# Kernel tuning notes

Hardware: AMD Instinct MI355X
Metric: run time of the kernel (lower is better)

## Reference

```python
import jax, jax.numpy as jnp
import numpy as np

INPUT_DIM = 512
OUTPUT_DIM = 512
NUM_BASIS = 16
GRID_MIN, GRID_MAX = -2.0, 2.0
LN_EPS = 1e-5


def rbf_basis(x):
    # x: [batch, input_dim] -> [batch, input_dim, num_basis]
    centers = jnp.linspace(GRID_MIN, GRID_MAX, NUM_BASIS, dtype=x.dtype)  # [K]
    h = (GRID_MAX - GRID_MIN) / (NUM_BASIS - 1)
    z = (x[..., None] - centers) / h
    return jnp.exp(-(z * z))


def setup_inputs() -> dict:
    key = jax.random.key(0)
    k1, k2, k3 = jax.random.split(key, 3)
    x = jax.random.normal(k1, (4096, INPUT_DIM), dtype=jnp.float32)
    weights = jax.random.normal(k2, (OUTPUT_DIM, INPUT_DIM, NUM_BASIS), dtype=jnp.float32) * 0.1
    base_weights = jax.random.normal(k3, (OUTPUT_DIM, INPUT_DIM), dtype=jnp.float32) * 0.1
    ln_gamma = jnp.ones((OUTPUT_DIM,), dtype=jnp.float32)
    ln_beta = jnp.zeros((OUTPUT_DIM,), dtype=jnp.float32)
    return {"x": x, "weights": weights, "base_weights": base_weights,
            "ln_gamma": ln_gamma, "ln_beta": ln_beta}


def reference(x, weights, base_weights, ln_gamma, ln_beta):
    # per-edge basis expansion: [B, I, K]
    basis = rbf_basis(x)
    # fused contraction replacing the nested python loops:
    # out[b, j] = sum_{i,k} basis[b, i, k] * weights[j, i, k]
    out = jnp.einsum('bik,jik->bj', basis, weights)
    # residual base activation path
    out = out + jax.nn.silu(x) @ base_weights.T
    # layer norm over output_dim
    mean = jnp.mean(out, axis=-1, keepdims=True)
    var = jnp.var(out, axis=-1, keepdims=True)
    out = (out - mean) * jax.lax.rsqrt(var + LN_EPS) * ln_gamma + ln_beta
    return out
```

## Files before the change

kernel.cpp:

```cpp
#include <hip/hip_runtime.h>
#include <hip/hip_bf16.h>


typedef __bf16 bf16x8 __attribute__((ext_vector_type(8)));
typedef __bf16 bf16x4 __attribute__((ext_vector_type(4)));
typedef float  f32x4  __attribute__((ext_vector_type(4)));

#define KT 8704
#define SPLITS 8
#define KS (KT / SPLITS)
#define NT2 (KS / 64)
#define CPE (4096 * 512)
#define ATILE (256 * 64)

__device__ __forceinline__ void gll16(const __bf16* g, __bf16* l) {
    __builtin_amdgcn_global_load_lds(
        (const __attribute__((address_space(1))) void*)g,
        (__attribute__((address_space(3))) void*)l, 16, 0, 0);
}

__global__ void prep_AB(const float* __restrict__ x, const float* __restrict__ W,
                        const float* __restrict__ Wb, __bf16* __restrict__ Asilu,
                        __bf16* __restrict__ B) {
    if (blockIdx.x < 1024) {
        int t = blockIdx.x * 256 + threadIdx.x;
        int e = t * 8;
        float4 v0 = *(const float4*)&x[e];
        float4 v1 = *(const float4*)&x[e + 4];
        float vs[8] = {v0.x, v0.y, v0.z, v0.w, v1.x, v1.y, v1.z, v1.w};
        bf16x8 o;
#pragma unroll
        for (int j = 0; j < 8; ++j) o[j] = (__bf16)(vs[j] / (1.0f + __expf(-vs[j])));
        *(bf16x8*)&Asilu[e] = o;
    } else {
        int t = (blockIdx.x - 1024) * 256 + threadIdx.x;
        int j = t / 2176;
        int c = (t - j * 2176) * 4;
        float4 v;
        if (c < 8192) v = *(const float4*)&W[(size_t)j * 8192 + c];
        else          v = *(const float4*)&Wb[(size_t)j * 512 + (c - 8192)];
        bf16x4 o;
        o[0] = (__bf16)v.x; o[1] = (__bf16)v.y; o[2] = (__bf16)v.z; o[3] = (__bf16)v.w;
        *(bf16x4*)&B[(size_t)j * KT + c] = o;
    }
}

__global__ __launch_bounds__(512, 2) void gemm_bt(const float* __restrict__ xg,
                                                  const __bf16* __restrict__ Sg,
                                                  const __bf16* __restrict__ B,
                                                  __bf16* __restrict__ Cp) {
    __shared__ __attribute__((aligned(16))) __bf16 As[2 * ATILE];
    __shared__ __attribute__((aligned(16))) __bf16 Bs[2 * ATILE];

    const int tid  = threadIdx.x;
    const int wave = tid >> 6, lane = tid & 63;
    const int q    = lane >> 4, r16 = lane & 15;
    const int m0 = blockIdx.x * 256, n0 = blockIdx.y * 256, k0 = blockIdx.z * KS;
    const int wm = wave >> 2, wn = wave & 3;

    const int sr = tid >> 3;
    const int sc = (tid & 7) ^ ((tid >> 4) & 7);
    const __bf16* gB0 = B + (size_t)(n0 + sr) * KT       + k0 + sc * 8;
    const __bf16* gB1 = B + (size_t)(n0 + 64  + sr) * KT + k0 + sc * 8;
    const __bf16* gB2 = B + (size_t)(n0 + 128 + sr) * KT + k0 + sc * 8;
    const __bf16* gB3 = B + (size_t)(n0 + 192 + sr) * KT + k0 + sc * 8;
    const __bf16* gS0 = Sg + (size_t)(m0 + sr) * 512       + sc * 8;
    const __bf16* gS1 = Sg + (size_t)(m0 + 64  + sr) * 512 + sc * 8;
    const __bf16* gS2 = Sg + (size_t)(m0 + 128 + sr) * 512 + sc * 8;
    const __bf16* gS3 = Sg + (size_t)(m0 + 192 + sr) * 512 + sc * 8;
    const float* xp0 = xg + (size_t)(m0 + sr) * 512       + (sc >> 1);
    const float* xp1 = xg + (size_t)(m0 + 64  + sr) * 512 + (sc >> 1);
    const float* xp2 = xg + (size_t)(m0 + 128 + sr) * 512 + (sc >> 1);
    const float* xp3 = xg + (size_t)(m0 + 192 + sr) * 512 + (sc >> 1);
    const float j0f  = (float)(8 * (sc & 1));

    f32x4 acc[8][4] = {};

    const int swl = (r16 >> 1) & 7;
    const int qx0 = ((q)     ^ swl) * 8;
    const int qx1 = ((4 + q) ^ swl) * 8;
    const int aro = (wm * 128 + r16) * 64;
    const int bro = (wn * 64  + r16) * 64;

    auto basis8 = [&](float xv) -> bf16x8 {
        const float zc = 3.75f * xv + 7.5f - j0f;
        bf16x8 o;
#pragma unroll
        for (int d = 0; d < 8; ++d) { float z = zc - (float)d; o[d] = (__bf16)__expf(-z * z); }
        return o;
    };

    float xA, xB, xC, xD;
    {
        const int xo = k0 >> 4;
        float x0 = xp0[xo], x1 = xp1[xo], x2 = xp2[xo], x3 = xp3[xo];
        gll16(gB0, &Bs[(size_t)tid * 8]);
        gll16(gB1, &Bs[(size_t)(512 + tid) * 8]);
        gll16(gB2, &Bs[(size_t)(1024 + tid) * 8]);
        gll16(gB3, &Bs[(size_t)(1536 + tid) * 8]);
        *(bf16x8*)(As + (size_t)tid * 8)          = basis8(x0);
        *(bf16x8*)(As + (size_t)(512 + tid) * 8)  = basis8(x1);
        *(bf16x8*)(As + (size_t)(1024 + tid) * 8) = basis8(x2);
        *(bf16x8*)(As + (size_t)(1536 + tid) * 8) = basis8(x3);
        const int xo1 = (k0 + 64) >> 4;
        xA = xp0[xo1]; xB = xp1[xo1]; xC = xp2[xo1]; xD = xp3[xo1];
    }
    __syncthreads();

    bf16x8 a[8], b[4];
    for (int u = 0; u < NT2; ++u) {
        const int s   = u & 1;
        const int cbo = s * ATILE;
        const int so1 = (s ^ 1) * ATILE;
        const int k1  = (u + 1) * 64;
        const int kn  = k0 + k1;
        const bool nb = kn < 8192;
        const int kk  = kn - 8192;
        const int k2g = kn + 64;
        const bool nb2 = k2g < 8192;
        float t0, t1, t2, t3;

#pragma unroll
        for (int mi = 0; mi < 8; ++mi) a[mi] = *(const bf16x8*)(As + cbo + aro + mi * 1024 + qx0);
#pragma unroll
        for (int ni = 0; ni < 4; ++ni) b[ni] = *(const bf16x8*)(Bs + cbo + bro + ni * 1024 + qx0);
        gll16(gB0 + k1, &Bs[(size_t)(so1 + tid * 8)]);
        gll16(gB1 + k1, &Bs[(size_t)(so1 + (512 + tid) * 8)]);
        gll16(gB2 + k1, &Bs[(size_t)(so1 + (1024 + tid) * 8)]);
        gll16(gB3 + k1, &Bs[(size_t)(so1 + (1536 + tid) * 8)]);
        if (nb) {
            *(bf16x8*)(As + so1 + (size_t)tid * 8)          = basis8(xA);
            *(bf16x8*)(As + so1 + (size_t)(1024 + tid) * 8) = basis8(xC);
        } else {
            gll16(gS0 + kk, &As[(size_t)(so1 + tid * 8)]);
            gll16(gS1 + kk, &As[(size_t)(so1 + (512 + tid) * 8)]);
            gll16(gS2 + kk, &As[(size_t)(so1 + (1024 + tid) * 8)]);
            gll16(gS3 + kk, &As[(size_t)(so1 + (1536 + tid) * 8)]);
        }
        if (nb2) {
            const int xo = k2g >> 4;
            t0 = xp0[xo]; t1 = xp1[xo]; t2 = xp2[xo]; t3 = xp3[xo];
        }
        __builtin_amdgcn_s_setprio(1);
#pragma unroll
        for (int mi = 0; mi < 8; ++mi)
#pragma unroll
            for (int ni = 0; ni < 4; ++ni)
                acc[mi][ni] = __builtin_amdgcn_mfma_f32_16x16x32_bf16(a[mi], b[ni], acc[mi][ni], 0, 0, 0);
        __builtin_amdgcn_s_setprio(0);
        __builtin_amdgcn_s_barrier();

#pragma unroll
        for (int mi = 0; mi < 8; ++mi) a[mi] = *(const bf16x8*)(As + cbo + aro + mi * 1024 + qx1);
#pragma unroll
        for (int ni = 0; ni < 4; ++ni) b[ni] = *(const bf16x8*)(Bs + cbo + bro + ni * 1024 + qx1);
        if (nb) {
            *(bf16x8*)(As + so1 + (size_t)(512 + tid) * 8)  = basis8(xB);
            *(bf16x8*)(As + so1 + (size_t)(1536 + tid) * 8) = basis8(xD);
        }
        __builtin_amdgcn_s_setprio(1);
#pragma unroll
        for (int mi = 0; mi < 8; ++mi)
#pragma unroll
            for (int ni = 0; ni < 4; ++ni)
                acc[mi][ni] = __builtin_amdgcn_mfma_f32_16x16x32_bf16(a[mi], b[ni], acc[mi][ni], 0, 0, 0);
        __builtin_amdgcn_s_setprio(0);
        if (nb2) { xA = t0; xB = t1; xC = t2; xD = t3; }
        __syncthreads();
    }

    __bf16* Cb = Cp + (size_t)blockIdx.z * CPE;
#pragma unroll
    for (int mi = 0; mi < 8; ++mi) {
        const int row = m0 + wm * 128 + mi * 16 + q * 4;
#pragma unroll
        for (int ni = 0; ni < 4; ++ni) {
            const int col = n0 + wn * 64 + ni * 16 + r16;
#pragma unroll
            for (int r = 0; r < 4; ++r)
                Cb[(size_t)(row + r) * 512 + col] = (__bf16)acc[mi][ni][r];
        }
    }
}

__global__ void ln_kernel(const __bf16* __restrict__ Cp, const float* __restrict__ gamma,
                          const float* __restrict__ beta, float* __restrict__ out) {
    const int tid  = threadIdx.x;
    const int wave = tid >> 6, lane = tid & 63;
    const int row  = blockIdx.x * 4 + wave;
    const size_t base = (size_t)row * 512 + lane * 8;

    float v[8] = {};
    float s = 0.f, s2 = 0.f;
#pragma unroll
    for (int z = 0; z < SPLITS; ++z) {
        bf16x8 p = *(const bf16x8*)(Cp + (size_t)z * CPE + base);
#pragma unroll
        for (int j = 0; j < 8; ++j) v[j] += (float)p[j];
    }
#pragma unroll
    for (int j = 0; j < 8; ++j) { s += v[j]; s2 += v[j] * v[j]; }
#pragma unroll
    for (int m = 32; m >= 1; m >>= 1) {
        s  += __shfl_xor(s, m);
        s2 += __shfl_xor(s2, m);
    }
    const float mean = s * (1.0f / 512.0f);
    const float var  = s2 * (1.0f / 512.0f) - mean * mean;
    const float rs   = rsqrtf(var + 1e-5f);
    float4 o0, o1;
    const float4 g0 = *(const float4*)&gamma[lane * 8];
    const float4 g1 = *(const float4*)&gamma[lane * 8 + 4];
    const float4 b0 = *(const float4*)&beta[lane * 8];
    const float4 b1 = *(const float4*)&beta[lane * 8 + 4];
    o0.x = (v[0] - mean) * rs * g0.x + b0.x;
    o0.y = (v[1] - mean) * rs * g0.y + b0.y;
    o0.z = (v[2] - mean) * rs * g0.z + b0.z;
    o0.w = (v[3] - mean) * rs * g0.w + b0.w;
    o1.x = (v[4] - mean) * rs * g1.x + b1.x;
    o1.y = (v[5] - mean) * rs * g1.y + b1.y;
    o1.z = (v[6] - mean) * rs * g1.z + b1.z;
    o1.w = (v[7] - mean) * rs * g1.w + b1.w;
    *(float4*)&out[base]     = o0;
    *(float4*)&out[base + 4] = o1;
}

extern "C" void kernel_launch(void* const* d_in, const int* in_sizes, int n_in,
                              void* d_out, int out_size, void* d_ws, size_t ws_size,
                              hipStream_t stream) {
    const float* x     = (const float*)d_in[0];
    const float* W     = (const float*)d_in[1];
    const float* Wb    = (const float*)d_in[2];
    const float* gamma = (const float*)d_in[3];
    const float* beta  = (const float*)d_in[4];
    float* out = (float*)d_out;

    char* ws = (char*)d_ws;
    __bf16* Asilu = (__bf16*)ws;
    __bf16* Bm    = (__bf16*)(ws + 4194304);
    __bf16* Cp    = (__bf16*)(ws + 13107200);

    prep_AB<<<1024 + 4352, 256, 0, stream>>>(x, W, Wb, Asilu, Bm);
    dim3 g(16, 2, SPLITS);
    gemm_bt<<<g, 512, 0, stream>>>(x, Asilu, Bm, Cp);
    ln_kernel<<<1024, 256, 0, stream>>>(Cp, gamma, beta, out);
}
```

Baseline: 129.6 us.

## Fuse SiLU computation into GEMM A-tile loading and drop precomputed SiLU buffer

The prep kernel no longer writes a bf16 SiLU copy of x. The GEMM instead loads fp32 x directly for the last 512 K columns and computes SiLU while staging the A tile into shared memory. The intra-iteration schedule also changes: the mid-iteration barrier is removed, and all A-tile writes move after the second-half fragment loads. This saves a kernel pass and a workspace round trip, at the cost of extra register pressure and exp work inside the GEMM. Dropping the barrier may be unsafe if other waves still read the buffer being overwritten.

```diff
diff --git a/kernel.cpp b/kernel.cpp
--- a/kernel.cpp
+++ b/kernel.cpp
@@ -19,34 +19,20 @@
         (__attribute__((address_space(3))) void*)l, 16, 0, 0);
 }
 
-__global__ void prep_AB(const float* __restrict__ x, const float* __restrict__ W,
-                        const float* __restrict__ Wb, __bf16* __restrict__ Asilu,
-                        __bf16* __restrict__ B) {
-    if (blockIdx.x < 1024) {
-        int t = blockIdx.x * 256 + threadIdx.x;
-        int e = t * 8;
-        float4 v0 = *(const float4*)&x[e];
-        float4 v1 = *(const float4*)&x[e + 4];
-        float vs[8] = {v0.x, v0.y, v0.z, v0.w, v1.x, v1.y, v1.z, v1.w};
-        bf16x8 o;
-#pragma unroll
-        for (int j = 0; j < 8; ++j) o[j] = (__bf16)(vs[j] / (1.0f + __expf(-vs[j])));
-        *(bf16x8*)&Asilu[e] = o;
-    } else {
-        int t = (blockIdx.x - 1024) * 256 + threadIdx.x;
-        int j = t / 2176;
-        int c = (t - j * 2176) * 4;
-        float4 v;
-        if (c < 8192) v = *(const float4*)&W[(size_t)j * 8192 + c];
-        else          v = *(const float4*)&Wb[(size_t)j * 512 + (c - 8192)];
-        bf16x4 o;
-        o[0] = (__bf16)v.x; o[1] = (__bf16)v.y; o[2] = (__bf16)v.z; o[3] = (__bf16)v.w;
-        *(bf16x4*)&B[(size_t)j * KT + c] = o;
-    }
+__global__ void prep_B(const float* __restrict__ W, const float* __restrict__ Wb,
+                       __bf16* __restrict__ B) {
+    int t = blockIdx.x * 256 + threadIdx.x;
+    int j = t / 2176;
+    int c = (t - j * 2176) * 4;
+    float4 v;
+    if (c < 8192) v = *(const float4*)&W[(size_t)j * 8192 + c];
+    else          v = *(const float4*)&Wb[(size_t)j * 512 + (c - 8192)];
+    bf16x4 o;
+    o[0] = (__bf16)v.x; o[1] = (__bf16)v.y; o[2] = (__bf16)v.z; o[3] = (__bf16)v.w;
+    *(bf16x4*)&B[(size_t)j * KT + c] = o;
 }
 
 __global__ __launch_bounds__(512, 2) void gemm_bt(const float* __restrict__ xg,
-                                                  const __bf16* __restrict__ Sg,
                                                   const __bf16* __restrict__ B,
                                                   __bf16* __restrict__ Cp) {
     __shared__ __attribute__((aligned(16))) __bf16 As[2 * ATILE];
@@ -64,15 +50,12 @@
     const __bf16* gB1 = B + (size_t)(n0 + 64  + sr) * KT + k0 + sc * 8;
     const __bf16* gB2 = B + (size_t)(n0 + 128 + sr) * KT + k0 + sc * 8;
     const __bf16* gB3 = B + (size_t)(n0 + 192 + sr) * KT + k0 + sc * 8;
-    const __bf16* gS0 = Sg + (size_t)(m0 + sr) * 512       + sc * 8;
-    const __bf16* gS1 = Sg + (size_t)(m0 + 64  + sr) * 512 + sc * 8;
-    const __bf16* gS2 = Sg + (size_t)(m0 + 128 + sr) * 512 + sc * 8;
-    const __bf16* gS3 = Sg + (size_t)(m0 + 192 + sr) * 512 + sc * 8;
-    const float* xp0 = xg + (size_t)(m0 + sr) * 512       + (sc >> 1);
-    const float* xp1 = xg + (size_t)(m0 + 64  + sr) * 512 + (sc >> 1);
-    const float* xp2 = xg + (size_t)(m0 + 128 + sr) * 512 + (sc >> 1);
-    const float* xp3 = xg + (size_t)(m0 + 192 + sr) * 512 + (sc >> 1);
-    const float j0f  = (float)(8 * (sc & 1));
+    const float* xs0 = xg + (size_t)(m0 + sr) * 512;
+    const float* xs1 = xg + (size_t)(m0 + 64  + sr) * 512;
+    const float* xs2 = xg + (size_t)(m0 + 128 + sr) * 512;
+    const float* xs3 = xg + (size_t)(m0 + 192 + sr) * 512;
+    const int   xco = sc >> 1;
+    const float j0f = (float)(8 * (sc & 1));
 
     f32x4 acc[8][4] = {};
 
@@ -89,11 +72,18 @@
         for (int d = 0; d < 8; ++d) { float z = zc - (float)d; o[d] = (__bf16)__expf(-z * z); }
         return o;
     };
+    auto silu8 = [&](float4 va, float4 vb) -> bf16x8 {
+        float v[8] = {va.x, va.y, va.z, va.w, vb.x, vb.y, vb.z, vb.w};
+        bf16x8 o;
+#pragma unroll
+        for (int d = 0; d < 8; ++d) o[d] = (__bf16)(v[d] / (1.0f + __expf(-v[d])));
+        return o;
+    };
 
     float xA, xB, xC, xD;
     {
-        const int xo = k0 >> 4;
-        float x0 = xp0[xo], x1 = xp1[xo], x2 = xp2[xo], x3 = xp3[xo];
+        const int xo = (k0 >> 4) + xco;
+        float x0 = xs0[xo], x1 = xs1[xo], x2 = xs2[xo], x3 = xs3[xo];
         gll16(gB0, &Bs[(size_t)tid * 8]);
         gll16(gB1, &Bs[(size_t)(512 + tid) * 8]);
         gll16(gB2, &Bs[(size_t)(1024 + tid) * 8]);
@@ -102,8 +92,8 @@
         *(bf16x8*)(As + (size_t)(512 + tid) * 8)  = basis8(x1);
         *(bf16x8*)(As + (size_t)(1024 + tid) * 8) = basis8(x2);
         *(bf16x8*)(As + (size_t)(1536 + tid) * 8) = basis8(x3);
-        const int xo1 = (k0 + 64) >> 4;
-        xA = xp0[xo1]; xB = xp1[xo1]; xC = xp2[xo1]; xD = xp3[xo1];
+        const int xo1 = ((k0 + 64) >> 4) + xco;
+        xA = xs0[xo1]; xB = xs1[xo1]; xC = xs2[xo1]; xD = xs3[xo1];
     }
     __syncthreads();
 
@@ -115,10 +105,11 @@
         const int k1  = (u + 1) * 64;
         const int kn  = k0 + k1;
         const bool nb = kn < 8192;
-        const int kk  = kn - 8192;
+        const int kk  = (kn - 8192 > 448) ? 448 : (kn - 8192);
         const int k2g = kn + 64;
         const bool nb2 = k2g < 8192;
         float t0, t1, t2, t3;
+        float4 sa0, sa1, sb0, sb1, sc0, sc1, sd0, sd1;
 
 #pragma unroll
         for (int mi = 0; mi < 8; ++mi) a[mi] = *(const bf16x8*)(As + cbo + aro + mi * 1024 + qx0);
@@ -128,35 +119,39 @@
         gll16(gB1 + k1, &Bs[(size_t)(so1 + (512 + tid) * 8)]);
         gll16(gB2 + k1, &Bs[(size_t)(so1 + (1024 + tid) * 8)]);
         gll16(gB3 + k1, &Bs[(size_t)(so1 + (1536 + tid) * 8)]);
+        if (!nb) {
+            const int col = kk + sc * 8;
+            sa0 = *(const float4*)(xs0 + col); sa1 = *(const float4*)(xs0 + col + 4);
+            sb0 = *(const float4*)(xs1 + col); sb1 = *(const float4*)(xs1 + col + 4);
+            sc0 = *(const float4*)(xs2 + col); sc1 = *(const float4*)(xs2 + col + 4);
+            sd0 = *(const float4*)(xs3 + col); sd1 = *(const float4*)(xs3 + col + 4);
+        }
+        if (nb2) {
+            const int xo = (k2g >> 4) + xco;
+            t0 = xs0[xo]; t1 = xs1[xo]; t2 = xs2[xo]; t3 = xs3[xo];
+        }
+        __builtin_amdgcn_s_setprio(1);
+#pragma unroll
+        for (int mi = 0; mi < 8; ++mi)
+#pragma unroll
+            for (int ni = 0; ni < 4; ++ni)
+                acc[mi][ni] = __builtin_amdgcn_mfma_f32_16x16x32_bf16(a[mi], b[ni], acc[mi][ni], 0, 0, 0);
+        __builtin_amdgcn_s_setprio(0);
+
+#pragma unroll
+        for (int mi = 0; mi < 8; ++mi) a[mi] = *(const bf16x8*)(As + cbo + aro + mi * 1024 + qx1);
+#pragma unroll
+        for (int ni = 0; ni < 4; ++ni) b[ni] = *(const bf16x8*)(Bs + cbo + bro + ni * 1024 + qx1);
         if (nb) {
             *(bf16x8*)(As + so1 + (size_t)tid * 8)          = basis8(xA);
             *(bf16x8*)(As + so1 + (size_t)(1024 + tid) * 8) = basis8(xC);
-        } else {
-            gll16(gS0 + kk, &As[(size_t)(so1 + tid * 8)]);
-            gll16(gS1 + kk, &As[(size_t)(so1 + (512 + tid) * 8)]);
-            gll16(gS2 + kk, &As[(size_t)(so1 + (1024 + tid) * 8)]);
-            gll16(gS3 + kk, &As[(size_t)(so1 + (1536 + tid) * 8)]);
-        }
-        if (nb2) {
-            const int xo = k2g >> 4;
-            t0 = xp0[xo]; t1 = xp1[xo]; t2 = xp2[xo]; t3 = xp3[xo];
-        }
-        __builtin_amdgcn_s_setprio(1);
-#pragma unroll
-        for (int mi = 0; mi < 8; ++mi)
-#pragma unroll
-            for (int ni = 0; ni < 4; ++ni)
-                acc[mi][ni] = __builtin_amdgcn_mfma_f32_16x16x32_bf16(a[mi], b[ni], acc[mi][ni], 0, 0, 0);
-        __builtin_amdgcn_s_setprio(0);
-        __builtin_amdgcn_s_barrier();
-
-#pragma unroll
-        for (int mi = 0; mi < 8; ++mi) a[mi] = *(const bf16x8*)(As + cbo + aro + mi * 1024 + qx1);
-#pragma unroll
-        for (int ni = 0; ni < 4; ++ni) b[ni] = *(const bf16x8*)(Bs + cbo + bro + ni * 1024 + qx1);
-        if (nb) {
             *(bf16x8*)(As + so1 + (size_t)(512 + tid) * 8)  = basis8(xB);
             *(bf16x8*)(As + so1 + (size_t)(1536 + tid) * 8) = basis8(xD);
+        } else {
+            *(bf16x8*)(As + so1 + (size_t)tid * 8)          = silu8(sa0, sa1);
+            *(bf16x8*)(As + so1 + (size_t)(512 + tid) * 8)  = silu8(sb0, sb1);
+            *(bf16x8*)(As + so1 + (size_t)(1024 + tid) * 8) = silu8(sc0, sc1);
+            *(bf16x8*)(As + so1 + (size_t)(1536 + tid) * 8) = silu8(sd0, sd1);
         }
         __builtin_amdgcn_s_setprio(1);
 #pragma unroll
@@ -236,12 +231,11 @@
     float* out = (float*)d_out;
 
     char* ws = (char*)d_ws;
-    __bf16* Asilu = (__bf16*)ws;
-    __bf16* Bm    = (__bf16*)(ws + 4194304);
-    __bf16* Cp    = (__bf16*)(ws + 13107200);
-
-    prep_AB<<<1024 + 4352, 256, 0, stream>>>(x, W, Wb, Asilu, Bm);
+    __bf16* Bm = (__bf16*)ws;
+    __bf16* Cp = (__bf16*)(ws + 8912896);
+
+    prep_B<<<4352, 256, 0, stream>>>(W, Wb, Bm);
     dim3 g(16, 2, SPLITS);
-    gemm_bt<<<g, 512, 0, stream>>>(x, Asilu, Bm, Cp);
+    gemm_bt<<<g, 512, 0, stream>>>(x, Bm, Cp);
     ln_kernel<<<1024, 256, 0, stream>>>(Cp, gamma, beta, out);
 }
```

Result: slower. 140.8 us (+8.6%).
